# Kernel tuning notes

Measured on AMD Instinct MI355X. Metric: run time of the kernel, lower is better.

Reference implementation:

```python
import jax, jax.numpy as jnp
import numpy as np

H = 1024  # hidden_size
N = 2 * H # encoder feature dim


def setup_inputs() -> dict:
    key = jax.random.key(0)
    ks = jax.random.split(key, 8)
    T, B = 2048, 16
    dec = jax.random.normal(ks[0], (B, H), dtype=jnp.float32)
    enc = jax.random.normal(ks[1], (T, B, N), dtype=jnp.float32)
    mask = jax.random.randint(ks[2], (T, B), 0, 2) > 0
    cov = jax.random.uniform(ks[3], (T, B), dtype=jnp.float32)
    # parameters (PyTorch Linear convention: y = x @ W.T + b)
    Wd = jax.random.normal(ks[4], (N, H), dtype=jnp.float32) / np.sqrt(H)
    bd = jnp.zeros((N,), dtype=jnp.float32)
    wc = jax.random.normal(ks[5], (N,), dtype=jnp.float32)  # coverage_projection: Linear(1, N, bias=False)
    v = jax.random.normal(ks[6], (N,), dtype=jnp.float32) / np.sqrt(N)  # v: Linear(N, 1, bias=False)
    return {"decoder_hidden_states": dec, "encoder_outs": enc,
            "encoder_padding_mask": mask, "coverage": cov,
            "Wd": Wd, "bd": bd, "wc": wc, "v": v}


def reference(decoder_hidden_states, encoder_outs, encoder_padding_mask, coverage, Wd, bd, wc, v):
    # dec_fea: [B, N]
    dec_fea = decoder_hidden_states @ Wd.T + bd
    # att_features: [T, B, N] = enc + broadcast dec + coverage feature
    att = encoder_outs + dec_fea[None, :, :] + coverage[:, :, None] * wc[None, None, :]
    e = jnp.tanh(att)
    # attn_scores: [T, B] via matvec with v
    scores = jnp.einsum('tbn,n->tb', e, v)
    scores = jnp.where(encoder_padding_mask, -jnp.inf, scores)
    attn_dist = jax.nn.softmax(scores, axis=0)  # softmax over T
    # context: [B, N]
    c = jnp.einsum('tb,tbn->bn', attn_dist, encoder_outs)
    coverage_out = coverage + attn_dist
    return (c, attn_dist, coverage_out)
```

## Files before the change

kernel.cpp:

```cpp
#include <hip/hip_runtime.h>


#define HH 1024
#define NNF 2048
#define TTT 2048
#define BB 16
#define NCHUNK 64
#define RPW 8

#define WS_DECFEA 0
#define WS_P      (BB * NNF)
#define WS_LPART  (WS_P + TTT * BB)
#define WS_CPART  (WS_LPART + NCHUNK * BB)

__device__ __forceinline__ float tanh_fast(float x) {
    float e = __expf(2.0f * x);
    return 1.0f - 2.0f * __builtin_amdgcn_rcpf(e + 1.0f);
}

__global__ __launch_bounds__(256) void k_decfea(const float* __restrict__ dec,
                                                const float* __restrict__ Wd,
                                                const float* __restrict__ bd,
                                                float* __restrict__ dec_fea) {
    const int n    = (blockIdx.x * 256 + threadIdx.x) >> 6;
    const int lane = threadIdx.x & 63;
    const float* wr = Wd + (size_t)n * HH;

    float acc[BB];
#pragma unroll
    for (int b = 0; b < BB; ++b) acc[b] = 0.0f;

#pragma unroll
    for (int it = 0; it < 4; ++it) {
        const int h = it * 256 + lane * 4;
        const float4 w4 = *(const float4*)(wr + h);
#pragma unroll
        for (int b = 0; b < BB; ++b) {
            const float4 d4 = *(const float4*)(dec + b * HH + h);
            acc[b] = fmaf(w4.x, d4.x, acc[b]);
            acc[b] = fmaf(w4.y, d4.y, acc[b]);
            acc[b] = fmaf(w4.z, d4.z, acc[b]);
            acc[b] = fmaf(w4.w, d4.w, acc[b]);
        }
    }
#pragma unroll
    for (int b = 0; b < BB; ++b) {
#pragma unroll
        for (int off = 32; off; off >>= 1) acc[b] += __shfl_xor(acc[b], off, 64);
    }
    if (lane == 0) {
        const float bias = bd[n];
#pragma unroll
        for (int b = 0; b < BB; ++b) dec_fea[b * NNF + n] = acc[b] + bias;
    }
}

__global__ __launch_bounds__(256, 2) void k_main(const float* __restrict__ enc,
                                                 const int* __restrict__ mask,
                                                 const float* __restrict__ cov,
                                                 const float* __restrict__ wc,
                                                 const float* __restrict__ v,
                                                 float* __restrict__ ws) {
    const int b     = blockIdx.y;
    const int chunk = blockIdx.x;
    const int tid   = threadIdx.x;
    const int lane  = tid & 63;
    const int w     = tid >> 6;
    const int t0    = chunk * (4 * RPW) + w * RPW;
    const int nb    = lane * 4;

    const float* dec_fea = ws + WS_DECFEA;
    float* ws_p     = ws + WS_P;
    float* ws_lpart = ws + WS_LPART;
    float* cpart    = ws + WS_CPART;

    float4 d[8], wv[8], vv[8], c[8];
#pragma unroll
    for (int s = 0; s < 8; ++s) {
        const int n = s * 256 + nb;
        d[s]  = *(const float4*)(dec_fea + b * NNF + n);
        wv[s] = *(const float4*)(wc + n);
        vv[s] = *(const float4*)(v + n);
        c[s]  = make_float4(0.f, 0.f, 0.f, 0.f);
    }

    float l_loc = 0.0f;

    float4 f[8];
    {
        const float* row = enc + ((size_t)t0 * BB + b) * NNF;
#pragma unroll
        for (int s = 0; s < 8; ++s) f[s] = *(const float4*)(row + s * 256 + nb);
    }

#pragma unroll
    for (int r = 0; r < RPW; ++r) {
        const int t = t0 + r;
        float4 fn[8];
        if (r + 1 < RPW) {
            const float* rowN = enc + ((size_t)(t + 1) * BB + b) * NNF;
#pragma unroll
            for (int s = 0; s < 8; ++s) fn[s] = *(const float4*)(rowN + s * 256 + nb);
        }
        const float cv = cov[t * BB + b];

        float sa = 0.0f;
#pragma unroll
        for (int s = 0; s < 8; ++s) {
            float a;
            a = fmaf(cv, wv[s].x, f[s].x + d[s].x); sa = fmaf(tanh_fast(a), vv[s].x, sa);
            a = fmaf(cv, wv[s].y, f[s].y + d[s].y); sa = fmaf(tanh_fast(a), vv[s].y, sa);
            a = fmaf(cv, wv[s].z, f[s].z + d[s].z); sa = fmaf(tanh_fast(a), vv[s].z, sa);
            a = fmaf(cv, wv[s].w, f[s].w + d[s].w); sa = fmaf(tanh_fast(a), vv[s].w, sa);
        }
#pragma unroll
        for (int off = 32; off; off >>= 1) sa += __shfl_xor(sa, off, 64);

        const bool pad = mask[t * BB + b] != 0;
        const float p = pad ? 0.0f : __expf(sa);
        l_loc += p;
#pragma unroll
        for (int s = 0; s < 8; ++s) {
            c[s].x = fmaf(p, f[s].x, c[s].x);
            c[s].y = fmaf(p, f[s].y, c[s].y);
            c[s].z = fmaf(p, f[s].z, c[s].z);
            c[s].w = fmaf(p, f[s].w, c[s].w);
        }
        if (lane == 0) ws_p[t * BB + b] = p;
#pragma unroll
        for (int s = 0; s < 8; ++s) f[s] = fn[s];
    }

    __shared__ float cbuf[4][NNF];
    __shared__ float lred[4];
#pragma unroll
    for (int s = 0; s < 8; ++s) *(float4*)(&cbuf[w][s * 256 + nb]) = c[s];
    if (lane == 0) lred[w] = l_loc;
    __syncthreads();

    float* cp = cpart + (size_t)(chunk * BB + b) * NNF;
#pragma unroll
    for (int half = 0; half < 2; ++half) {
        const int e = half * 1024 + tid * 4;
        float4 s0 = *(const float4*)(&cbuf[0][e]);
        float4 s1 = *(const float4*)(&cbuf[1][e]);
        float4 s2 = *(const float4*)(&cbuf[2][e]);
        float4 s3 = *(const float4*)(&cbuf[3][e]);
        float4 o;
        o.x = (s0.x + s1.x) + (s2.x + s3.x);
        o.y = (s0.y + s1.y) + (s2.y + s3.y);
        o.z = (s0.z + s1.z) + (s2.z + s3.z);
        o.w = (s0.w + s1.w) + (s2.w + s3.w);
        *(float4*)(cp + e) = o;
    }
    if (tid == 0)
        ws_lpart[chunk * BB + b] = (lred[0] + lred[1]) + (lred[2] + lred[3]);
}

__global__ __launch_bounds__(256) void k_fin(const float* __restrict__ ws,
                                             const float* __restrict__ cov,
                                             float* __restrict__ out_c,
                                             float* __restrict__ out_attn,
                                             float* __restrict__ out_cov) {
    const int tid = threadIdx.x;
    __shared__ float pr[16][17];
    __shared__ float linv[16];
    {
        const int bb = tid & 15;
        const int g  = tid >> 4;
        float s = 0.0f;
#pragma unroll
        for (int k = 0; k < 4; ++k)
            s += ws[WS_LPART + (g * 4 + k) * BB + bb];
        pr[g][bb] = s;
    }
    __syncthreads();
    if (tid < 16) {
        float tot = 0.0f;
#pragma unroll
        for (int g = 0; g < 16; ++g) tot += pr[g][tid];
        linv[tid] = 1.0f / tot;
    }
    __syncthreads();

    if (blockIdx.x < 32) {
        const int k = blockIdx.x;
        const int b = k >> 1;
        const int n = (k & 1) * 1024 + tid * 4;
        float4 s = {0.f, 0.f, 0.f, 0.f};
#pragma unroll 8
        for (int j = 0; j < NCHUNK; ++j) {
            const float4 a = *(const float4*)(ws + WS_CPART + (size_t)(j * BB + b) * NNF + n);
            s.x += a.x; s.y += a.y; s.z += a.z; s.w += a.w;
        }
        const float li = linv[b];
        s.x *= li; s.y *= li; s.z *= li; s.w *= li;
        *(float4*)(out_c + b * NNF + n) = s;
    } else {
        const int idx = (blockIdx.x - 32) * 256 + tid;
        const int b = idx & (BB - 1);
        const float a = ws[WS_P + idx] * linv[b];
        out_attn[idx] = a;
        out_cov[idx] = cov[idx] + a;
    }
}

extern "C" void kernel_launch(void* const* d_in, const int* in_sizes, int n_in,
                              void* d_out, int out_size, void* d_ws, size_t ws_size,
                              hipStream_t stream) {
    const float* dec  = (const float*)d_in[0];
    const float* enc  = (const float*)d_in[1];
    const int*   mask = (const int*)d_in[2];
    const float* cov  = (const float*)d_in[3];
    const float* Wd   = (const float*)d_in[4];
    const float* bd   = (const float*)d_in[5];
    const float* wc   = (const float*)d_in[6];
    const float* v    = (const float*)d_in[7];
    float* ws  = (float*)d_ws;
    float* out = (float*)d_out;

    float* out_c    = out;
    float* out_attn = out + BB * NNF;
    float* out_cov  = out_attn + TTT * BB;

    k_decfea<<<512, 256, 0, stream>>>(dec, Wd, bd, ws + WS_DECFEA);

    dim3 g2(NCHUNK, BB);
    k_main<<<g2, 256, 0, stream>>>(enc, mask, cov, wc, v, ws);

    k_fin<<<160, 256, 0, stream>>>(ws, cov, out_c, out_attn, out_cov);
}
```

Before: 436.5 us.

## Stage dec_fea/wc/v in LDS, drop register prefetch, raise occupancy to 3

```diff
diff --git a/kernel.cpp b/kernel.cpp
--- a/kernel.cpp
+++ b/kernel.cpp
@@ -12,6 +12,8 @@
 #define WS_P      (BB * NNF)
 #define WS_LPART  (WS_P + TTT * BB)
 #define WS_CPART  (WS_LPART + NCHUNK * BB)
+
+typedef float fx4 __attribute__((ext_vector_type(4)));
 
 __device__ __forceinline__ float tanh_fast(float x) {
     float e = __expf(2.0f * x);
@@ -55,7 +57,7 @@
     }
 }
 
-__global__ __launch_bounds__(256, 2) void k_main(const float* __restrict__ enc,
+__global__ __launch_bounds__(256, 3) void k_main(const float* __restrict__ enc,
                                                  const int* __restrict__ mask,
                                                  const float* __restrict__ cov,
                                                  const float* __restrict__ wc,
@@ -66,58 +68,58 @@
     const int tid   = threadIdx.x;
     const int lane  = tid & 63;
     const int w     = tid >> 6;
-    const int t0    = chunk * (4 * RPW) + w * RPW;
     const int nb    = lane * 4;
 
-    const float* dec_fea = ws + WS_DECFEA;
+    __shared__ float smem[4 * NNF];
+    __shared__ float lred[4];
+
     float* ws_p     = ws + WS_P;
     float* ws_lpart = ws + WS_LPART;
     float* cpart    = ws + WS_CPART;
 
-    float4 d[8], wv[8], vv[8], c[8];
-#pragma unroll
-    for (int s = 0; s < 8; ++s) {
-        const int n = s * 256 + nb;
-        d[s]  = *(const float4*)(dec_fea + b * NNF + n);
-        wv[s] = *(const float4*)(wc + n);
-        vv[s] = *(const float4*)(v + n);
-        c[s]  = make_float4(0.f, 0.f, 0.f, 0.f);
-    }
-
+    {
+        const float* dec_fea = ws + WS_DECFEA + b * NNF;
+#pragma unroll
+        for (int i = tid * 4; i < NNF; i += 1024) {
+            *(float4*)&smem[i]            = *(const float4*)(dec_fea + i);
+            *(float4*)&smem[NNF + i]      = *(const float4*)(wc + i);
+            *(float4*)&smem[2 * NNF + i]  = *(const float4*)(v + i);
+        }
+    }
+    __syncthreads();
+
+    fx4 c[8];
+#pragma unroll
+    for (int s = 0; s < 8; ++s) c[s] = (fx4)0.0f;
     float l_loc = 0.0f;
 
-    float4 f[8];
-    {
-        const float* row = enc + ((size_t)t0 * BB + b) * NNF;
-#pragma unroll
-        for (int s = 0; s < 8; ++s) f[s] = *(const float4*)(row + s * 256 + nb);
-    }
-
-#pragma unroll
+    const int tbase = chunk * (4 * RPW) + w * RPW;
+
     for (int r = 0; r < RPW; ++r) {
-        const int t = t0 + r;
-        float4 fn[8];
-        if (r + 1 < RPW) {
-            const float* rowN = enc + ((size_t)(t + 1) * BB + b) * NNF;
-#pragma unroll
-            for (int s = 0; s < 8; ++s) fn[s] = *(const float4*)(rowN + s * 256 + nb);
-        }
+        const int t = tbase + r;
+        const float* row = enc + ((size_t)t * BB + b) * NNF + nb;
+        fx4 f[8];
+#pragma unroll
+        for (int s = 0; s < 8; ++s)
+            f[s] = __builtin_nontemporal_load((const fx4*)(row + s * 256));
         const float cv = cov[t * BB + b];
 
         float sa = 0.0f;
 #pragma unroll
         for (int s = 0; s < 8; ++s) {
+            const fx4 dd = *(const fx4*)&smem[s * 256 + nb];
+            const fx4 ww = *(const fx4*)&smem[NNF + s * 256 + nb];
+            const fx4 vx = *(const fx4*)&smem[2 * NNF + s * 256 + nb];
             float a;
-            a = fmaf(cv, wv[s].x, f[s].x + d[s].x); sa = fmaf(tanh_fast(a), vv[s].x, sa);
-            a = fmaf(cv, wv[s].y, f[s].y + d[s].y); sa = fmaf(tanh_fast(a), vv[s].y, sa);
-            a = fmaf(cv, wv[s].z, f[s].z + d[s].z); sa = fmaf(tanh_fast(a), vv[s].z, sa);
-            a = fmaf(cv, wv[s].w, f[s].w + d[s].w); sa = fmaf(tanh_fast(a), vv[s].w, sa);
+            a = fmaf(cv, ww.x, f[s].x + dd.x); sa = fmaf(tanh_fast(a), vx.x, sa);
+            a = fmaf(cv, ww.y, f[s].y + dd.y); sa = fmaf(tanh_fast(a), vx.y, sa);
+            a = fmaf(cv, ww.z, f[s].z + dd.z); sa = fmaf(tanh_fast(a), vx.z, sa);
+            a = fmaf(cv, ww.w, f[s].w + dd.w); sa = fmaf(tanh_fast(a), vx.w, sa);
         }
 #pragma unroll
         for (int off = 32; off; off >>= 1) sa += __shfl_xor(sa, off, 64);
 
-        const bool pad = mask[t * BB + b] != 0;
-        const float p = pad ? 0.0f : __expf(sa);
+        const float p = (mask[t * BB + b] != 0) ? 0.0f : __expf(sa);
         l_loc += p;
 #pragma unroll
         for (int s = 0; s < 8; ++s) {
@@ -127,14 +129,11 @@
             c[s].w = fmaf(p, f[s].w, c[s].w);
         }
         if (lane == 0) ws_p[t * BB + b] = p;
-#pragma unroll
-        for (int s = 0; s < 8; ++s) f[s] = fn[s];
-    }
-
-    __shared__ float cbuf[4][NNF];
-    __shared__ float lred[4];
-#pragma unroll
-    for (int s = 0; s < 8; ++s) *(float4*)(&cbuf[w][s * 256 + nb]) = c[s];
+    }
+
+    __syncthreads();
+#pragma unroll
+    for (int s = 0; s < 8; ++s) *(fx4*)&smem[w * NNF + s * 256 + nb] = c[s];
     if (lane == 0) lred[w] = l_loc;
     __syncthreads();
 
@@ -142,16 +141,12 @@
 #pragma unroll
     for (int half = 0; half < 2; ++half) {
         const int e = half * 1024 + tid * 4;
-        float4 s0 = *(const float4*)(&cbuf[0][e]);
-        float4 s1 = *(const float4*)(&cbuf[1][e]);
-        float4 s2 = *(const float4*)(&cbuf[2][e]);
-        float4 s3 = *(const float4*)(&cbuf[3][e]);
-        float4 o;
-        o.x = (s0.x + s1.x) + (s2.x + s3.x);
-        o.y = (s0.y + s1.y) + (s2.y + s3.y);
-        o.z = (s0.z + s1.z) + (s2.z + s3.z);
-        o.w = (s0.w + s1.w) + (s2.w + s3.w);
-        *(float4*)(cp + e) = o;
+        fx4 s0 = *(const fx4*)&smem[0 * NNF + e];
+        fx4 s1 = *(const fx4*)&smem[1 * NNF + e];
+        fx4 s2 = *(const fx4*)&smem[2 * NNF + e];
+        fx4 s3 = *(const fx4*)&smem[3 * NNF + e];
+        fx4 o = (s0 + s1) + (s2 + s3);
+        *(fx4*)(cp + e) = o;
     }
     if (tid == 0)
         ws_lpart[chunk * BB + b] = (lred[0] + lred[1]) + (lred[2] + lred[3]);
```

Result: faster. 409.1 us (-6.3%).
